# Kernel optimization log

Measured on AMD Instinct MI355X. Metric: run time of the kernel, lower is better.

The kernel has to match this reference:

```python
import jax, jax.numpy as jnp
import numpy as np

N = 50000   # nodes
E = 800000  # edges
IN = 128    # in_channels
H = 256     # hidden_channels
G = 128     # graphs in batch
NEG_SLOPE = 0.2


def _gat_conv(x, src, dst, W, a_src, a_dst, b):
    # PyG GATConv, heads=1: xp = W x; e_ij = LeakyReLU(a_src.xp_j + a_dst.xp_i);
    # softmax over incoming edges of target i; out_i = sum_j alpha_ij xp_j + b
    xp = x @ W                                   # [N, H]
    e = jax.nn.leaky_relu(xp[src] @ a_src + xp[dst] @ a_dst, NEG_SLOPE)  # [Et]
    m = jax.ops.segment_max(e, dst, num_segments=N)
    m = jnp.where(jnp.isfinite(m), m, 0.0)
    p = jnp.exp(e - m[dst])
    denom = jax.ops.segment_sum(p, dst, num_segments=N)
    alpha = p / denom[dst]
    return jax.ops.segment_sum(alpha[:, None] * xp[src], dst, num_segments=N) + b


def _gru_step_h0(x, W_ih, W_hh, b_ih, b_hh):
    # torch.nn.GRU, seq_len=1, h0=0. Gate order: r, z, n.
    gi = x @ W_ih.T + b_ih                       # [N, 3H]
    i_r, i_z, i_n = jnp.split(gi, 3, axis=-1)
    h_r, h_z, h_n = jnp.split(b_hh, 3)           # h0=0 -> hidden gates are biases
    r = jax.nn.sigmoid(i_r + h_r)
    z = jax.nn.sigmoid(i_z + h_z)
    n = jnp.tanh(i_n + r * h_n)
    return (1.0 - z) * n                         # + z * h0 (=0)


def setup_inputs() -> dict:
    key = jax.random.key(0)
    ks = jax.random.split(key, 18)
    s = 0.05
    inp = {
        "x": jax.random.normal(ks[0], (N, IN), jnp.float32),
        "edge_index": jax.random.randint(ks[1], (2, E), 0, N, dtype=jnp.int32).astype(jnp.int64),
        "batch": jnp.sort(jax.random.randint(ks[2], (N,), 0, G, dtype=jnp.int32)).astype(jnp.int64),
        # GAT layer 0 (in->H) and layer 1 (H->H)
        "W0": jax.random.normal(ks[3], (IN, H), jnp.float32) * s,
        "a_src0": jax.random.normal(ks[4], (H,), jnp.float32) * s,
        "a_dst0": jax.random.normal(ks[5], (H,), jnp.float32) * s,
        "b0": jnp.zeros((H,), jnp.float32),
        "W1": jax.random.normal(ks[6], (H, H), jnp.float32) * s,
        "a_src1": jax.random.normal(ks[7], (H,), jnp.float32) * s,
        "a_dst1": jax.random.normal(ks[8], (H,), jnp.float32) * s,
        "b1": jnp.zeros((H,), jnp.float32),
        # GRU(H, H)
        "W_ih": jax.random.normal(ks[9], (3 * H, H), jnp.float32) * s,
        "W_hh": jax.random.normal(ks[10], (3 * H, H), jnp.float32) * s,
        "b_ih": jnp.zeros((3 * H,), jnp.float32),
        "b_hh": jnp.zeros((3 * H,), jnp.float32),
        # super_node_fc
        "Wf": jax.random.normal(ks[11], (H, H), jnp.float32) * s,
        "bf": jnp.zeros((H,), jnp.float32),
    }
    return inp


def reference(x, edge_index, batch, W0, a_src0, a_dst0, b0, W1, a_src1, a_dst1, b1,
              W_ih, W_hh, b_ih, b_hh, Wf, bf):
    # add self loops (PyG GATConv default)
    loops = jnp.arange(N, dtype=edge_index.dtype)
    src = jnp.concatenate([edge_index[0], loops])
    dst = jnp.concatenate([edge_index[1], loops])

    h = jax.nn.relu(_gat_conv(x, src, dst, W0, a_src0, a_dst0, b0))  # dropout=identity (eval)
    h = jax.nn.relu(_gat_conv(h, src, dst, W1, a_src1, a_dst1, b1))

    h = _gru_step_h0(h, W_ih, W_hh, b_ih, b_hh)                      # [N, H]

    h = jax.ops.segment_sum(h, batch, num_segments=G)                # global_add_pool [G, H]
    super_node = jnp.mean(h, axis=0, keepdims=True)                  # [1, H]
    super_node = jax.nn.relu(super_node @ Wf.T + bf)
    return jnp.concatenate([h, jnp.broadcast_to(super_node, (G, H))], axis=1)  # [G, 2H]
```

## Files before the change

kernel.cpp:

```cpp
#include <hip/hip_runtime.h>
#include <hip/hip_fp16.h>
#include <math.h>

#define N_NODES 50000
#define N_PAD   50176
#define N_EDGES 800000
#define ET (N_EDGES + N_NODES)
#define IN_CH 128
#define H 256
#define G_GRAPHS 128
#define NEG_SLOPE 0.2f
#define GRU_CHUNK 25000
#define NB 391

typedef __attribute__((ext_vector_type(8))) short short8;
typedef __attribute__((ext_vector_type(4))) float f32x4;
typedef __attribute__((ext_vector_type(2))) float f32x2;
typedef unsigned short u16;
typedef unsigned char u8;

#if __has_builtin(__builtin_amdgcn_cvt_f32_fp8) && __has_builtin(__builtin_amdgcn_cvt_pk_fp8_f32)
#define USE_FP8_BUILTINS 1
#else
#define USE_FP8_BUILTINS 0
#endif
#if USE_FP8_BUILTINS && __has_builtin(__builtin_amdgcn_cvt_pk_f32_fp8)
#define HAVE_PK_DEC 1
#else
#define HAVE_PK_DEC 0
#endif

__device__ inline u16 f2bf(float v) {
    unsigned u = __float_as_uint(v);
    unsigned r = (u + 0x7FFFu + ((u >> 16) & 1u)) >> 16;
    return (u16)r;
}
__device__ inline float bf2f(u16 v) {
    return __uint_as_float(((unsigned)v) << 16);
}

#if USE_FP8_BUILTINS
#define FP8_WSCALE 1.0f
__device__ inline u8 fp8_enc(float v) {
    int r = __builtin_amdgcn_cvt_pk_fp8_f32(v, v, 0, false);
    return (u8)(r & 0xFF);
}
__device__ inline void fp8_dec4(unsigned rv, float& f0, float& f1, float& f2, float& f3) {
#if HAVE_PK_DEC
    f32x2 lo = __builtin_amdgcn_cvt_pk_f32_fp8((int)rv, false);
    f32x2 hi = __builtin_amdgcn_cvt_pk_f32_fp8((int)rv, true);
    f0 = lo.x; f1 = lo.y; f2 = hi.x; f3 = hi.y;
#else
    f0 = __builtin_amdgcn_cvt_f32_fp8((int)rv, 0);
    f1 = __builtin_amdgcn_cvt_f32_fp8((int)rv, 1);
    f2 = __builtin_amdgcn_cvt_f32_fp8((int)rv, 2);
    f3 = __builtin_amdgcn_cvt_f32_fp8((int)rv, 3);
#endif
}
#else
#define FP8_WSCALE 256.0f
__device__ inline u8 fp8_enc(float f) {
    unsigned u = __float_as_uint(f);
    unsigned s = (u >> 31) << 7;
    float a = fabsf(f);
    if (a >= 448.f) return (u8)(s | 0x7E);
    unsigned bits = __float_as_uint(a);
    int exp = (int)((bits >> 23) & 255) - 127;
    unsigned m23 = bits & 0x7fffff;
    if (exp < -6) {
        int m = (int)rintf(a * 512.f);
        if (m >= 8) return (u8)(s | (1 << 3));
        return (u8)(s | m);
    }
    int e8 = exp + 7;
    unsigned m = m23 >> 20, rem = m23 & 0xFFFFF;
    if (rem > 0x80000 || (rem == 0x80000 && (m & 1))) m++;
    if (m == 8) { m = 0; e8++; }
    if (e8 > 15 || (e8 == 15 && m == 7)) return (u8)(s | 0x7E);
    return (u8)(s | (e8 << 3) | m);
}
__device__ inline void fp8_dec4(unsigned rv, float& f0, float& f1, float& f2, float& f3) {
    unsigned hA = ((rv & 0x00800080u) << 8) | ((rv & 0x007f007fu) << 7);
    unsigned rs = rv >> 8;
    unsigned hB = ((rs & 0x00800080u) << 8) | ((rs & 0x007f007fu) << 7);
    __half2 a = *(__half2*)&hA;
    __half2 b = *(__half2*)&hB;
    f0 = __low2float(a);  f2 = __high2float(a);
    f1 = __low2float(b);  f3 = __high2float(b);
}
#endif

__device__ inline void async_cp16(const u16* g, u16* l) {
    __builtin_amdgcn_global_load_lds(
        (const __attribute__((address_space(1))) unsigned int*)g,
        (__attribute__((address_space(3))) unsigned int*)l,
        16, 0, 0);
}

__global__ __launch_bounds__(256) void bucket_hist(const int* __restrict__ ei,
                                                   int* __restrict__ gcnt) {
    __shared__ int h[NB];
    int t = threadIdx.x;
    for (int b = t; b < NB; b += 256) h[b] = 0;
    __syncthreads();
    for (int e = blockIdx.x * 256 + t; e < N_EDGES; e += gridDim.x * 256)
        atomicAdd(&h[ei[N_EDGES + e] >> 7], 1);
    __syncthreads();
    for (int b = t; b < NB; b += 256)
        if (h[b]) atomicAdd(&gcnt[b], h[b]);
}

__global__ __launch_bounds__(512) void bucket_scan(const int* __restrict__ gcnt,
                                                   int* __restrict__ off,
                                                   int* __restrict__ cur) {
    __shared__ int s[NB + 1];
    int t = threadIdx.x;
    if (t < NB) s[t] = gcnt[t];
    __syncthreads();
    if (t == 0) {
        int a = 0;
        for (int b = 0; b < NB; b++) { int c = s[b]; s[b] = a; a += c; }
        s[NB] = a;
    }
    __syncthreads();
    if (t <= NB) { off[t] = s[t]; if (t < NB) cur[t] = s[t]; }
}

#define EPT 16
__global__ __launch_bounds__(256) void bucket_scatter(const int* __restrict__ ei,
                                                      int* __restrict__ bucketCur,
                                                      int2* __restrict__ rec) {
    __shared__ int cnt[NB];
    __shared__ int base[NB];
    int t = threadIdx.x;
    for (int b = t; b < NB; b += 256) cnt[b] = 0;
    __syncthreads();
    int e0 = blockIdx.x * (256 * EPT);
    int sa[EPT], da[EPT], rk[EPT];
#pragma unroll
    for (int k = 0; k < EPT; k++) {
        int e = e0 + k * 256 + t;
        if (e < N_EDGES) {
            sa[k] = ei[e];
            da[k] = ei[N_EDGES + e];
            rk[k] = atomicAdd(&cnt[da[k] >> 7], 1);
        }
    }
    __syncthreads();
    for (int b = t; b < NB; b += 256) {
        int c = cnt[b];
        base[b] = c ? atomicAdd(&bucketCur[b], c) : 0;
    }
    __syncthreads();
#pragma unroll
    for (int k = 0; k < EPT; k++) {
        int e = e0 + k * 256 + t;
        if (e < N_EDGES) rec[base[da[k] >> 7] + rk[k]] = make_int2(sa[k], da[k]);
    }
}

__global__ __launch_bounds__(256) void build_csr(const int2* __restrict__ rec,
                                                 const int* __restrict__ off,
                                                 int* __restrict__ indptr,
                                                 int* __restrict__ eidsSrc) {
    __shared__ int cnt[128];
    __shared__ int scn[128];
    __shared__ int cur[128];
    int b = blockIdx.x, t = threadIdx.x;
    int nInB = N_NODES - b * 128;
    if (nInB > 128) nInB = 128;
    if (t < 128) cnt[t] = 0;
    __syncthreads();
    int lo = off[b], hi = off[b + 1];
    for (int i = lo + t; i < hi; i += 256) atomicAdd(&cnt[rec[i].y & 127], 1);
    __syncthreads();
    if (t < 128) scn[t] = cnt[t] + 1;
    __syncthreads();
    for (int o = 1; o < 128; o <<= 1) {
        int v = 0;
        if (t < 128 && t >= o) v = scn[t - o];
        __syncthreads();
        if (t < 128 && t >= o) scn[t] += v;
        __syncthreads();
    }
    int base = off[b] + 128 * b;
    if (t < nInB) {
        int start = base + (t ? scn[t - 1] : 0);
        int node = b * 128 + t;
        indptr[node] = start;
        eidsSrc[start] = node;
        cur[t] = start + 1;
    }
    if (b == 0 && t == 0) indptr[N_NODES] = ET;
    __syncthreads();
    for (int i = lo + t; i < hi; i += 256) {
        int2 r = rec[i];
        int pos = atomicAdd(&cur[r.y & 127], 1);
        eidsSrc[pos] = r.x;
    }
}

__global__ __launch_bounds__(256) void prep_kernel(const float* __restrict__ x,
                                                   const float* __restrict__ Wih,
                                                   const float* __restrict__ W0,
                                                   const float* __restrict__ W1,
                                                   u16* __restrict__ x_bf,
                                                   u16* __restrict__ Wih_bf,
                                                   u16* __restrict__ W0t,
                                                   u16* __restrict__ W1t) {
    int i = blockIdx.x * 256 + threadIdx.x;
    int seg = blockIdx.y;
    if (seg == 0) {
        if (i < N_NODES * IN_CH / 4) {
            float4 v = *(const float4*)&x[i * 4];
            ushort4 o = {f2bf(v.x), f2bf(v.y), f2bf(v.z), f2bf(v.w)};
            *(ushort4*)&x_bf[i * 4] = o;
        }
    } else if (seg == 1) {
        if (i < 3 * H * H / 4) {
            float4 v = *(const float4*)&Wih[i * 4];
            ushort4 o = {f2bf(v.x), f2bf(v.y), f2bf(v.z), f2bf(v.w)};
            *(ushort4*)&Wih_bf[i * 4] = o;
        }
    } else if (seg == 2) {
        if (i < IN_CH * H) {
            int k = i / H, n = i % H;
            W0t[(size_t)n * IN_CH + k] = f2bf(W0[i]);
        }
    } else {
        if (i < H * H) {
            int k = i / H, n = i % H;
            W1t[(size_t)n * H + k] = f2bf(W1[i]);
        }
    }
}

struct StageMem { u16 As[128][32]; u16 Bs[256][32]; };
struct EpiMem   { u8 xt[128][256]; float rS[4][64]; float rD[4][64]; };
union ShMem     { StageMem s; EpiMem e; };

template <bool FUSE>
__global__ __launch_bounds__(256, 2) void gemm_wide(const u16* __restrict__ A,
                                                    const u16* __restrict__ Bt,
                                                    u16* __restrict__ C,
                                                    u8* __restrict__ C8,
                                                    const float* __restrict__ avS,
                                                    const float* __restrict__ avD,
                                                    float* __restrict__ sS,
                                                    float* __restrict__ sD,
                                                    int M, int K, int Ntot) {
    __shared__ ShMem shm;
    int t = threadIdx.x;
    int m0 = blockIdx.x * 128;
    int n0 = blockIdx.y * 256;
    int wave = t >> 6, lane = t & 63;
    int wm = (wave >> 1) * 64, wn = (wave & 1) * 128;
    int lrow = lane & 15;
    int lq = lane >> 4;

    f32x4 acc[4][8];
#pragma unroll
    for (int i = 0; i < 4; i++)
#pragma unroll
        for (int j = 0; j < 8; j++)
            acc[i][j] = (f32x4){0.f, 0.f, 0.f, 0.f};

    int r0 = t >> 2, q0 = t & 3;
    const u16* gA0 = A + (size_t)(m0 + r0) * K + q0 * 8;
    const u16* gA1 = gA0 + (size_t)64 * K;
    const u16* gB0 = Bt + (size_t)(n0 + r0) * K + q0 * 8;
    const u16* gB1 = gB0 + (size_t)64 * K;
    const u16* gB2 = gB0 + (size_t)128 * K;
    const u16* gB3 = gB0 + (size_t)192 * K;
    u16* lA0 = &shm.s.As[0][0] + t * 8;
    u16* lA1 = lA0 + 256 * 8;
    u16* lB0 = &shm.s.Bs[0][0] + t * 8;
    u16* lB1 = lB0 + 256 * 8;
    u16* lB2 = lB0 + 512 * 8;
    u16* lB3 = lB0 + 768 * 8;

    for (int k0 = 0; k0 < K; k0 += 32) {
        __syncthreads();
        async_cp16(gA0 + k0, lA0);
        async_cp16(gA1 + k0, lA1);
        async_cp16(gB0 + k0, lB0);
        async_cp16(gB1 + k0, lB1);
        async_cp16(gB2 + k0, lB2);
        async_cp16(gB3 + k0, lB3);
        __syncthreads();
        short8 af[4], bfr[8];
#pragma unroll
        for (int i = 0; i < 4; i++)
            af[i] = *(const short8*)&shm.s.As[wm + i * 16 + lrow][lq * 8];
#pragma unroll
        for (int j = 0; j < 8; j++)
            bfr[j] = *(const short8*)&shm.s.Bs[wn + j * 16 + lrow][lq * 8];
#pragma unroll
        for (int i = 0; i < 4; i++)
#pragma unroll
            for (int j = 0; j < 8; j++)
                acc[i][j] = __builtin_amdgcn_mfma_f32_16x16x32_bf16(af[i], bfr[j], acc[i][j], 0, 0, 0);
    }

    if constexpr (FUSE) {
        __syncthreads();
        float aS[8], aD[8];
#pragma unroll
        for (int j = 0; j < 8; j++) {
            aS[j] = avS[wn + j * 16 + lrow];
            aD[j] = avD[wn + j * 16 + lrow];
        }
#pragma unroll
        for (int i = 0; i < 4; i++) {
#pragma unroll
            for (int reg = 0; reg < 4; reg++) {
                float ps = 0.f, pd = 0.f;
                int rloc = wm + i * 16 + lq * 4 + reg;
#pragma unroll
                for (int j = 0; j < 8; j++) {
                    float v = acc[i][j][reg];
                    ps += v * aS[j];
                    pd += v * aD[j];
                    shm.e.xt[rloc][wn + j * 16 + lrow] = fp8_enc(v);
                }
#pragma unroll
                for (int m = 1; m < 16; m <<= 1) {
                    ps += __shfl_xor(ps, m);
                    pd += __shfl_xor(pd, m);
                }
                if (lrow == 0) {
                    shm.e.rS[wave][i * 16 + lq * 4 + reg] = ps;
                    shm.e.rD[wave][i * 16 + lq * 4 + reg] = pd;
                }
            }
        }
        __syncthreads();
        if (t < 128) {
            int w0 = (t >> 6) << 1;
            int l = t & 63;
            int gm = m0 + t;
            if (gm < M) {
                sS[gm] = shm.e.rS[w0][l] + shm.e.rS[w0 + 1][l];
                sD[gm] = shm.e.rD[w0][l] + shm.e.rD[w0 + 1][l];
            }
        }
#pragma unroll
        for (int pass = 0; pass < 8; pass++) {
            int idx = pass * 256 + t;
            int row = idx >> 4;
            int c16 = (idx & 15) << 4;
            int4 vv = *(const int4*)&shm.e.xt[row][c16];
            *(int4*)&C8[(size_t)(m0 + row) * 256 + c16] = vv;
        }
    } else {
#pragma unroll
        for (int i = 0; i < 4; i++) {
#pragma unroll
            for (int reg = 0; reg < 4; reg++) {
                int gm = m0 + wm + i * 16 + lq * 4 + reg;
                if (gm < M) {
#pragma unroll
                    for (int j = 0; j < 8; j++) {
                        int gn = n0 + wn + j * 16 + lrow;
                        C[(size_t)gm * Ntot + gn] = f2bf(acc[i][j][reg]);
                    }
                }
            }
        }
    }
}

__global__ __launch_bounds__(256) void gat_agg_fp8(const u8* __restrict__ xp8,
                                                   const float* __restrict__ s_src,
                                                   const float* __restrict__ s_dst,
                                                   const int* __restrict__ indptr,
                                                   const int* __restrict__ eidsSrc,
                                                   const float* __restrict__ bias,
                                                   u16* __restrict__ out) {
    __shared__ int2 sSW[4][64];
    int wave = threadIdx.x >> 6, lane = threadIdx.x & 63;
    int n = blockIdx.x * 4 + wave;
    int start = indptr[n];
    int deg = indptr[n + 1] - start;
    float sdn = s_dst[n];
    int col = lane << 2;
    float a0 = 0.f, a1 = 0.f, a2 = 0.f, a3 = 0.f;

    if (deg <= 64) {
        int s = 0;
        float v = -1e30f;
        if (lane < deg) {
            s = eidsSrc[start + lane];
            float u = s_src[s] + sdn;
            v = (u >= 0.f) ? u : NEG_SLOPE * u;
        }
        float m = v;
#pragma unroll
        for (int off = 32; off; off >>= 1) m = fmaxf(m, __shfl_xor(m, off));
        float pw = (lane < deg) ? expf(v - m) : 0.f;
        float dsum = pw;
#pragma unroll
        for (int off = 32; off; off >>= 1) dsum += __shfl_xor(dsum, off);
        float w = pw * (FP8_WSCALE / dsum);
        sSW[wave][lane] = make_int2(s, __float_as_int(w));
        int j = 0;
        for (; j + 8 <= deg; j += 8) {
            unsigned rv[8];
            float wv[8];
#pragma unroll
            for (int k = 0; k < 8; k++) {
                int2 sw = sSW[wave][j + k];
                wv[k] = __int_as_float(sw.y);
                rv[k] = *(const unsigned*)&xp8[(size_t)sw.x * H + col];
            }
#pragma unroll
            for (int k = 0; k < 8; k++) {
                float f0, f1, f2, f3;
                fp8_dec4(rv[k], f0, f1, f2, f3);
                a0 += wv[k] * f0; a1 += wv[k] * f1;
                a2 += wv[k] * f2; a3 += wv[k] * f3;
            }
        }
        for (; j < deg; j++) {
            int2 sw = sSW[wave][j];
            float wj = __int_as_float(sw.y);
            unsigned rv = *(const unsigned*)&xp8[(size_t)sw.x * H + col];
            float f0, f1, f2, f3;
            fp8_dec4(rv, f0, f1, f2, f3);
            a0 += wj * f0; a1 += wj * f1; a2 += wj * f2; a3 += wj * f3;
        }
    } else {
        float m = -1e30f;
        for (int i = lane; i < deg; i += 64) {
            int s = eidsSrc[start + i];
            float u = s_src[s] + sdn;
            u = (u >= 0.f) ? u : NEG_SLOPE * u;
            m = fmaxf(m, u);
        }
#pragma unroll
        for (int off = 32; off; off >>= 1) m = fmaxf(m, __shfl_xor(m, off));
        float dsum = 0.f;
        for (int i = lane; i < deg; i += 64) {
            int s = eidsSrc[start + i];
            float u = s_src[s] + sdn;
            u = (u >= 0.f) ? u : NEG_SLOPE * u;
            dsum += expf(u - m);
        }
#pragma unroll
        for (int off = 32; off; off >>= 1) dsum += __shfl_xor(dsum, off);
        float dinv = FP8_WSCALE / dsum;
        for (int base = 0; base < deg; base += 64) {
            int cnt = min(64, deg - base);
            int s = 0; float w = 0.f;
            if (lane < cnt) {
                s = eidsSrc[start + base + lane];
                float u = s_src[s] + sdn;
                u = (u >= 0.f) ? u : NEG_SLOPE * u;
                w = expf(u - m) * dinv;
            }
            sSW[wave][lane] = make_int2(s, __float_as_int(w));
            for (int j = 0; j < cnt; j++) {
                int2 sw = sSW[wave][j];
                float wj = __int_as_float(sw.y);
                unsigned rv = *(const unsigned*)&xp8[(size_t)sw.x * H + col];
                float f0, f1, f2, f3;
                fp8_dec4(rv, f0, f1, f2, f3);
                a0 += wj * f0; a1 += wj * f1; a2 += wj * f2; a3 += wj * f3;
            }
        }
    }
    float4 bv = *(const float4*)&bias[col];
    ushort4 o;
    o.x = f2bf(fmaxf(a0 + bv.x, 0.f));
    o.y = f2bf(fmaxf(a1 + bv.y, 0.f));
    o.z = f2bf(fmaxf(a2 + bv.z, 0.f));
    o.w = f2bf(fmaxf(a3 + bv.w, 0.f));
    *(ushort4*)&out[(size_t)n * H + col] = o;
}

__global__ __launch_bounds__(256) void gru_gates_pool(const u16* __restrict__ gates,
                                                      const float* __restrict__ b_ih,
                                                      const float* __restrict__ b_hh,
                                                      const int* __restrict__ batch,
                                                      float* __restrict__ pooled,
                                                      int nodeBase, int nodeCount) {
    int t = threadIdx.x;
    int i0 = blockIdx.x * 16;
    if (i0 >= nodeCount) return;
    float bir = b_ih[t], biz = b_ih[256 + t], bin_ = b_ih[512 + t];
    float bhr = b_hh[t], bhz = b_hh[256 + t], bhn = b_hh[512 + t];
    int iend = min(16, nodeCount - i0);
    float acc = 0.f;
    int cur_g = batch[nodeBase + i0];
    for (int i = 0; i < iend; i++) {
        size_t row = (size_t)(i0 + i) * 768;
        float ir = bf2f(gates[row + t]);
        float iz = bf2f(gates[row + 256 + t]);
        float in_ = bf2f(gates[row + 512 + t]);
        float r = 1.f / (1.f + expf(-(ir + bir + bhr)));
        float z = 1.f / (1.f + expf(-(iz + biz + bhz)));
        float nn = tanhf(in_ + bin_ + r * bhn);
        float h = (1.f - z) * nn;
        int g = batch[nodeBase + i0 + i];
        if (g != cur_g) {
            atomicAdd(&pooled[(size_t)cur_g * H + t], acc);
            acc = 0.f;
            cur_g = g;
        }
        acc += h;
    }
    atomicAdd(&pooled[(size_t)cur_g * H + t], acc);
}

__global__ __launch_bounds__(256) void super_kernel(const float* __restrict__ pooled,
                                                    const float* __restrict__ Wf,
                                                    const float* __restrict__ bf,
                                                    float* __restrict__ sup) {
    __shared__ float smean[256];
    int t = threadIdx.x;
    float s = 0.f;
    for (int g = 0; g < G_GRAPHS; g++) s += pooled[(size_t)g * H + t];
    smean[t] = s / (float)G_GRAPHS;
    __syncthreads();
    float acc = 0.f;
    for (int k = 0; k < H; k++) acc += smean[k] * Wf[(size_t)t * H + k];
    acc += bf[t];
    sup[t] = fmaxf(acc, 0.f);
}

__global__ __launch_bounds__(256) void writeout(const float* __restrict__ pooled,
                                                const float* __restrict__ sup,
                                                float* __restrict__ out) {
    int idx = blockIdx.x * 256 + threadIdx.x;
    int g = idx >> 9, c = idx & 511;
    out[idx] = (c < H) ? pooled[(size_t)g * H + c] : sup[c - H];
}

extern "C" void kernel_launch(void* const* d_in, const int* in_sizes, int n_in,
                              void* d_out, int out_size, void* d_ws, size_t ws_size,
                              hipStream_t stream) {
    const float* x      = (const float*)d_in[0];
    const int*   ei     = (const int*)d_in[1];
    const int*   batch  = (const int*)d_in[2];
    const float* W0     = (const float*)d_in[3];
    const float* a_src0 = (const float*)d_in[4];
    const float* a_dst0 = (const float*)d_in[5];
    const float* b0     = (const float*)d_in[6];
    const float* W1     = (const float*)d_in[7];
    const float* a_src1 = (const float*)d_in[8];
    const float* a_dst1 = (const float*)d_in[9];
    const float* b1     = (const float*)d_in[10];
    const float* W_ih   = (const float*)d_in[11];
    const float* b_ih   = (const float*)d_in[13];
    const float* b_hh   = (const float*)d_in[14];
    const float* Wf     = (const float*)d_in[15];
    const float* bf     = (const float*)d_in[16];
    float* out = (float*)d_out;

    char* p = (char*)d_ws;
    auto alloc = [&](size_t bytes) -> void* {
        void* r = (void*)p;
        p += (bytes + 255) & ~(size_t)255;
        return r;
    };
    u16*   h_bf   = (u16*)alloc((size_t)N_PAD * H * 2);
    u16*   x_bf   = (u16*)alloc((size_t)N_PAD * IN_CH * 2);
    u8*    xp8    = (u8*)alloc((size_t)N_PAD * H);
    u16*   gatesC = (u16*)alloc((size_t)GRU_CHUNK * 3 * H * 2);
    u16*   W0t    = (u16*)alloc((size_t)H * IN_CH * 2);
    u16*   W1t    = (u16*)alloc((size_t)H * H * 2);
    u16*   Wih_bf = (u16*)alloc((size_t)3 * H * H * 2);
    float* s_src  = (float*)alloc((size_t)N_NODES * 4);
    float* s_dst  = (float*)alloc((size_t)N_NODES * 4);
    int2*  rec    = (int2*)alloc((size_t)N_EDGES * 8);
    int*   eidsSrc= (int*)alloc((size_t)ET * 4);
    int*   indptr = (int*)alloc((size_t)(N_NODES + 1) * 4);
    int*   gBkt   = (int*)alloc((size_t)(NB + 1) * 4);
    int*   bktOff = (int*)alloc((size_t)(NB + 1) * 4);
    int*   bktCur = (int*)alloc((size_t)(NB + 1) * 4);
    float* pooled = (float*)alloc((size_t)G_GRAPHS * H * 4);
    float* sup    = (float*)alloc((size_t)H * 4);

    hipMemsetAsync(gBkt, 0, (size_t)NB * 4, stream);
    bucket_hist<<<NB, 256, 0, stream>>>(ei, gBkt);
    bucket_scan<<<1, 512, 0, stream>>>(gBkt, bktOff, bktCur);
    bucket_scatter<<<(N_EDGES + 256 * EPT - 1) / (256 * EPT), 256, 0, stream>>>(ei, bktCur, rec);
    build_csr<<<NB, 256, 0, stream>>>(rec, bktOff, indptr, eidsSrc);

    prep_kernel<<<dim3((N_NODES * IN_CH / 4 + 255) / 256, 4), 256, 0, stream>>>(
        x, W_ih, W0, W1, x_bf, Wih_bf, W0t, W1t);

    const int MB = (N_NODES + 127) / 128;
    const int WB = N_NODES / 4;
    gemm_wide<true><<<dim3(MB, 1), 256, 0, stream>>>(
        x_bf, W0t, nullptr, xp8, a_src0, a_dst0, s_src, s_dst, N_NODES, IN_CH, H);
    gat_agg_fp8<<<WB, 256, 0, stream>>>(xp8, s_src, s_dst, indptr, eidsSrc, b0, h_bf);
    gemm_wide<true><<<dim3(MB, 1), 256, 0, stream>>>(
        h_bf, W1t, nullptr, xp8, a_src1, a_dst1, s_src, s_dst, N_NODES, H, H);
    gat_agg_fp8<<<WB, 256, 0, stream>>>(xp8, s_src, s_dst, indptr, eidsSrc, b1, h_bf);
    hipMemsetAsync(pooled, 0, (size_t)G_GRAPHS * H * 4, stream);
    for (int base = 0; base < N_NODES; base += GRU_CHUNK) {
        int cnt = min(GRU_CHUNK, N_NODES - base);
        gemm_wide<false><<<dim3((cnt + 127) / 128, 3), 256, 0, stream>>>(
            h_bf + (size_t)base * H, Wih_bf, gatesC, nullptr, nullptr, nullptr, nullptr, nullptr,
            cnt, H, 3 * H);
        gru_gates_pool<<<(cnt + 15) / 16, 256, 0, stream>>>(gatesC, b_ih, b_hh, batch, pooled, base, cnt);
    }
    super_kernel<<<1, 256, 0, stream>>>(pooled, Wf, bf, sup);
    writeout<<<(G_GRAPHS * 2 * H) / 256, 256, 0, stream>>>(pooled, sup, out);
}
```

Baseline: 422.0 us.

## Split GAT score epilogue into separate kernel and XOR-swizzle GEMM shared tiles

Removes the fused epilogue from the wide GEMM. The GEMM now writes a bf16 result. A new sdot_fp8 kernel then reads that result, computes the source and destination attention scores with a wave reduction, and writes packed 4-wide fp8 values. The GEMM also gains an XOR swizzle on the shared-memory tile columns to cut bank conflicts on the fragment reads, which benefits all GEMM launches. In exchange, each GAT layer writes and re-reads a full bf16 xp buffer and pays an extra kernel launch. The fp8 buffer now aliases the x_bf workspace.

```diff
diff --git a/kernel.cpp b/kernel.cpp
--- a/kernel.cpp
+++ b/kernel.cpp
@@ -41,9 +41,11 @@
 
 #if USE_FP8_BUILTINS
 #define FP8_WSCALE 1.0f
-__device__ inline u8 fp8_enc(float v) {
-    int r = __builtin_amdgcn_cvt_pk_fp8_f32(v, v, 0, false);
-    return (u8)(r & 0xFF);
+__device__ inline unsigned fp8_pack4(float a, float b, float c, float d) {
+    int v = 0;
+    v = __builtin_amdgcn_cvt_pk_fp8_f32(a, b, v, false);
+    v = __builtin_amdgcn_cvt_pk_fp8_f32(c, d, v, true);
+    return (unsigned)v;
 }
 __device__ inline void fp8_dec4(unsigned rv, float& f0, float& f1, float& f2, float& f3) {
 #if HAVE_PK_DEC
@@ -59,7 +61,7 @@
 }
 #else
 #define FP8_WSCALE 256.0f
-__device__ inline u8 fp8_enc(float f) {
+__device__ inline u8 fp8_enc1(float f) {
     unsigned u = __float_as_uint(f);
     unsigned s = (u >> 31) << 7;
     float a = fabsf(f);
@@ -78,6 +80,10 @@
     if (m == 8) { m = 0; e8++; }
     if (e8 > 15 || (e8 == 15 && m == 7)) return (u8)(s | 0x7E);
     return (u8)(s | (e8 << 3) | m);
+}
+__device__ inline unsigned fp8_pack4(float a, float b, float c, float d) {
+    return (unsigned)fp8_enc1(a) | ((unsigned)fp8_enc1(b) << 8) |
+           ((unsigned)fp8_enc1(c) << 16) | ((unsigned)fp8_enc1(d) << 24);
 }
 __device__ inline void fp8_dec4(unsigned rv, float& f0, float& f1, float& f2, float& f3) {
     unsigned hA = ((rv & 0x00800080u) << 8) | ((rv & 0x007f007fu) << 7);
@@ -235,21 +241,12 @@
     }
 }
 
-struct StageMem { u16 As[128][32]; u16 Bs[256][32]; };
-struct EpiMem   { u8 xt[128][256]; float rS[4][64]; float rD[4][64]; };
-union ShMem     { StageMem s; EpiMem e; };
-
-template <bool FUSE>
 __global__ __launch_bounds__(256, 2) void gemm_wide(const u16* __restrict__ A,
                                                     const u16* __restrict__ Bt,
                                                     u16* __restrict__ C,
-                                                    u8* __restrict__ C8,
-                                                    const float* __restrict__ avS,
-                                                    const float* __restrict__ avD,
-                                                    float* __restrict__ sS,
-                                                    float* __restrict__ sD,
                                                     int M, int K, int Ntot) {
-    __shared__ ShMem shm;
+    __shared__ u16 As[128][32];
+    __shared__ u16 Bs[256][32];
     int t = threadIdx.x;
     int m0 = blockIdx.x * 128;
     int n0 = blockIdx.y * 256;
@@ -265,19 +262,22 @@
         for (int j = 0; j < 8; j++)
             acc[i][j] = (f32x4){0.f, 0.f, 0.f, 0.f};
 
-    int r0 = t >> 2, q0 = t & 3;
-    const u16* gA0 = A + (size_t)(m0 + r0) * K + q0 * 8;
+    int r0 = t >> 2;
+    int qs = (t & 3) ^ ((t >> 3) & 3);
+    const u16* gA0 = A + (size_t)(m0 + r0) * K + qs * 8;
     const u16* gA1 = gA0 + (size_t)64 * K;
-    const u16* gB0 = Bt + (size_t)(n0 + r0) * K + q0 * 8;
+    const u16* gB0 = Bt + (size_t)(n0 + r0) * K + qs * 8;
     const u16* gB1 = gB0 + (size_t)64 * K;
     const u16* gB2 = gB0 + (size_t)128 * K;
     const u16* gB3 = gB0 + (size_t)192 * K;
-    u16* lA0 = &shm.s.As[0][0] + t * 8;
+    u16* lA0 = &As[0][0] + t * 8;
     u16* lA1 = lA0 + 256 * 8;
-    u16* lB0 = &shm.s.Bs[0][0] + t * 8;
+    u16* lB0 = &Bs[0][0] + t * 8;
     u16* lB1 = lB0 + 256 * 8;
     u16* lB2 = lB0 + 512 * 8;
     u16* lB3 = lB0 + 768 * 8;
+
+    int swz8 = (lq ^ ((lrow >> 1) & 3)) * 8;
 
     for (int k0 = 0; k0 < K; k0 += 32) {
         __syncthreads();
@@ -291,83 +291,54 @@
         short8 af[4], bfr[8];
 #pragma unroll
         for (int i = 0; i < 4; i++)
-            af[i] = *(const short8*)&shm.s.As[wm + i * 16 + lrow][lq * 8];
+            af[i] = *(const short8*)&As[wm + i * 16 + lrow][swz8];
 #pragma unroll
         for (int j = 0; j < 8; j++)
-            bfr[j] = *(const short8*)&shm.s.Bs[wn + j * 16 + lrow][lq * 8];
+            bfr[j] = *(const short8*)&Bs[wn + j * 16 + lrow][swz8];
 #pragma unroll
         for (int i = 0; i < 4; i++)
 #pragma unroll
             for (int j = 0; j < 8; j++)
                 acc[i][j] = __builtin_amdgcn_mfma_f32_16x16x32_bf16(af[i], bfr[j], acc[i][j], 0, 0, 0);
     }
-
-    if constexpr (FUSE) {
-        __syncthreads();
-        float aS[8], aD[8];
-#pragma unroll
-        for (int j = 0; j < 8; j++) {
-            aS[j] = avS[wn + j * 16 + lrow];
-            aD[j] = avD[wn + j * 16 + lrow];
-        }
-#pragma unroll
-        for (int i = 0; i < 4; i++) {
-#pragma unroll
-            for (int reg = 0; reg < 4; reg++) {
-                float ps = 0.f, pd = 0.f;
-                int rloc = wm + i * 16 + lq * 4 + reg;
+#pragma unroll
+    for (int i = 0; i < 4; i++) {
+#pragma unroll
+        for (int reg = 0; reg < 4; reg++) {
+            int gm = m0 + wm + i * 16 + lq * 4 + reg;
+            if (gm < M) {
 #pragma unroll
                 for (int j = 0; j < 8; j++) {
-                    float v = acc[i][j][reg];
-                    ps += v * aS[j];
-                    pd += v * aD[j];
-                    shm.e.xt[rloc][wn + j * 16 + lrow] = fp8_enc(v);
-                }
-#pragma unroll
-                for (int m = 1; m < 16; m <<= 1) {
-                    ps += __shfl_xor(ps, m);
-                    pd += __shfl_xor(pd, m);
-                }
-                if (lrow == 0) {
-                    shm.e.rS[wave][i * 16 + lq * 4 + reg] = ps;
-                    shm.e.rD[wave][i * 16 + lq * 4 + reg] = pd;
+                    int gn = n0 + wn + j * 16 + lrow;
+                    C[(size_t)gm * Ntot + gn] = f2bf(acc[i][j][reg]);
                 }
             }
         }
-        __syncthreads();
-        if (t < 128) {
-            int w0 = (t >> 6) << 1;
-            int l = t & 63;
-            int gm = m0 + t;
-            if (gm < M) {
-                sS[gm] = shm.e.rS[w0][l] + shm.e.rS[w0 + 1][l];
-                sD[gm] = shm.e.rD[w0][l] + shm.e.rD[w0 + 1][l];
-            }
-        }
-#pragma unroll
-        for (int pass = 0; pass < 8; pass++) {
-            int idx = pass * 256 + t;
-            int row = idx >> 4;
-            int c16 = (idx & 15) << 4;
-            int4 vv = *(const int4*)&shm.e.xt[row][c16];
-            *(int4*)&C8[(size_t)(m0 + row) * 256 + c16] = vv;
-        }
-    } else {
-#pragma unroll
-        for (int i = 0; i < 4; i++) {
-#pragma unroll
-            for (int reg = 0; reg < 4; reg++) {
-                int gm = m0 + wm + i * 16 + lq * 4 + reg;
-                if (gm < M) {
-#pragma unroll
-                    for (int j = 0; j < 8; j++) {
-                        int gn = n0 + wn + j * 16 + lrow;
-                        C[(size_t)gm * Ntot + gn] = f2bf(acc[i][j][reg]);
-                    }
-                }
-            }
-        }
-    }
+    }
+}
+
+__global__ __launch_bounds__(256) void sdot_fp8(const u16* __restrict__ xp,
+                                                const float* __restrict__ a_src,
+                                                const float* __restrict__ a_dst,
+                                                float* __restrict__ s_src,
+                                                float* __restrict__ s_dst,
+                                                u8* __restrict__ xp8) {
+    int wave = threadIdx.x >> 6, lane = threadIdx.x & 63;
+    int n = blockIdx.x * 4 + wave;
+    int col = lane << 2;
+    ushort4 v = *(const ushort4*)&xp[(size_t)n * H + col];
+    float4 a1 = *(const float4*)&a_src[col];
+    float4 a2 = *(const float4*)&a_dst[col];
+    float x0 = bf2f(v.x), x1 = bf2f(v.y), x2 = bf2f(v.z), x3 = bf2f(v.w);
+    *(unsigned*)&xp8[(size_t)n * H + col] = fp8_pack4(x0, x1, x2, x3);
+    float d1 = x0 * a1.x + x1 * a1.y + x2 * a1.z + x3 * a1.w;
+    float d2 = x0 * a2.x + x1 * a2.y + x2 * a2.z + x3 * a2.w;
+#pragma unroll
+    for (int off = 32; off; off >>= 1) {
+        d1 += __shfl_xor(d1, off);
+        d2 += __shfl_xor(d2, off);
+    }
+    if (lane == 0) { s_src[n] = d1; s_dst[n] = d2; }
 }
 
 __global__ __launch_bounds__(256) void gat_agg_fp8(const u8* __restrict__ xp8,
@@ -563,9 +534,10 @@
         p += (bytes + 255) & ~(size_t)255;
         return r;
     };
+    u16*   xp_bf  = (u16*)alloc((size_t)N_PAD * H * 2);
     u16*   h_bf   = (u16*)alloc((size_t)N_PAD * H * 2);
     u16*   x_bf   = (u16*)alloc((size_t)N_PAD * IN_CH * 2);
-    u8*    xp8    = (u8*)alloc((size_t)N_PAD * H);
+    u8*    xp8    = (u8*)x_bf;
     u16*   gatesC = (u16*)alloc((size_t)GRU_CHUNK * 3 * H * 2);
     u16*   W0t    = (u16*)alloc((size_t)H * IN_CH * 2);
     u16*   W1t    = (u16*)alloc((size_t)H * H * 2);
@@ -592,18 +564,17 @@
 
     const int MB = (N_NODES + 127) / 128;
     const int WB = N_NODES / 4;
-    gemm_wide<true><<<dim3(MB, 1), 256, 0, stream>>>(
-        x_bf, W0t, nullptr, xp8, a_src0, a_dst0, s_src, s_dst, N_NODES, IN_CH, H);
+    gemm_wide<<<dim3(MB, 1), 256, 0, stream>>>(x_bf, W0t, xp_bf, N_NODES, IN_CH, H);
+    sdot_fp8<<<WB, 256, 0, stream>>>(xp_bf, a_src0, a_dst0, s_src, s_dst, xp8);
     gat_agg_fp8<<<WB, 256, 0, stream>>>(xp8, s_src, s_dst, indptr, eidsSrc, b0, h_bf);
-    gemm_wide<true><<<dim3(MB, 1), 256, 0, stream>>>(
-        h_bf, W1t, nullptr, xp8, a_src1, a_dst1, s_src, s_dst, N_NODES, H, H);
+    gemm_wide<<<dim3(MB, 1), 256, 0, stream>>>(h_bf, W1t, xp_bf, N_NODES, H, H);
+    sdot_fp8<<<WB, 256, 0, stream>>>(xp_bf, a_src1, a_dst1, s_src, s_dst, xp8);
     gat_agg_fp8<<<WB, 256, 0, stream>>>(xp8, s_src, s_dst, indptr, eidsSrc, b1, h_bf);
     hipMemsetAsync(pooled, 0, (size_t)G_GRAPHS * H * 4, stream);
     for (int base = 0; base < N_NODES; base += GRU_CHUNK) {
         int cnt = min(GRU_CHUNK, N_NODES - base);
-        gemm_wide<false><<<dim3((cnt + 127) / 128, 3), 256, 0, stream>>>(
-            h_bf + (size_t)base * H, Wih_bf, gatesC, nullptr, nullptr, nullptr, nullptr, nullptr,
-            cnt, H, 3 * H);
+        gemm_wide<<<dim3((cnt + 127) / 128, 3), 256, 0, stream>>>(
+            h_bf + (size_t)base * H, Wih_bf, gatesC, cnt, H, 3 * H);
         gru_gates_pool<<<(cnt + 15) / 16, 256, 0, stream>>>(gatesC, b_ih, b_hh, batch, pooled, base, cnt);
     }
     super_kernel<<<1, 256, 0, stream>>>(pooled, Wf, bf, sup);
```

Result: faster. 373.6 us (-11.5%).
